# Kernel tuning notes

Measured on AMD Instinct MI355X. Metric: run time of the kernel, lower is better.

Reference implementation:

```python
import jax, jax.numpy as jnp
import numpy as np

B_, L_, H_, N_ = 8, 1024, 1024, 64

def setup_inputs() -> dict:
    key = jax.random.key(0)
    k1, k2, k3, k4 = jax.random.split(key, 4)
    return {
        "samples": jax.random.normal(k1, (B_, L_, 3 * H_), dtype=jnp.float32),
        "label_one_hot": jax.random.uniform(k2, (B_, L_, N_), dtype=jnp.float32),
        "predict": jax.random.normal(k3, (B_, L_, N_), dtype=jnp.float32),
        "W": jax.random.normal(k4, (H_, 3 * H_), dtype=jnp.float32) * (1.0 / np.sqrt(3 * H_)),
        "b_proj": jnp.zeros((H_,), dtype=jnp.float32),
    }

def reference(samples, label_one_hot, predict, W, b_proj):
    # projection: Linear(3H -> H)
    s = jnp.einsum("blk,hk->blh", samples, W) + b_proj          # [b,L,H]
    # dense similarity graph with diagonal masked out, row-softmax
    graph = jnp.einsum("blh,bmh->blm", s, s)                     # [b,L,L]
    L = graph.shape[1]
    eye = jnp.eye(L, dtype=graph.dtype)
    A = jax.nn.softmax(graph - 1e5 * eye, axis=-1)               # [b,L,L]
    # centered masked labels
    sup = label_one_hot
    row_has = (jnp.sum(sup, axis=-1) > 0.5).astype(sup.dtype)    # [b,L]
    total = jnp.sum(row_has, axis=-1)[:, None]                   # [b,1]
    avg = (jnp.sum(sup, axis=-2) / total)[:, None, :]            # [b,1,N]
    B0 = (sup - avg) * row_has[..., None]                        # [b,L,N]
    # diagonal inverse-degree scaling (elementwise, no dense diag matmul)
    d = 1.0 / (jnp.sum(A, axis=-1) + 1e-10)                      # [b,L]
    P = d[:, :, None] * jnp.swapaxes(A, -1, -2)                  # [b,L,L]
    Db = d[:, :, None] * B0                                      # [b,L,N]
    # 6-step power-iteration scan with residual injection at t==3
    ut = jnp.zeros_like(B0)
    for t in range(1, 7):
        ut = jnp.einsum("blm,bmn->bln", P, ut) + Db
        if t == 3:
            ut = ut + predict  # dropout is identity in eval mode
    return ut

if __name__ == "__main__":
    out = reference(**setup_inputs())
    print(out.shape, out.dtype)
```

## Files before the change

kernel.cpp:

```cpp
#include <hip/hip_runtime.h>


typedef _Float16 f16_t;
typedef f16_t f16x4 __attribute__((ext_vector_type(4)));
typedef f16_t f16x8 __attribute__((ext_vector_type(8)));
typedef float floatx4 __attribute__((ext_vector_type(4)));

__device__ __forceinline__ void async_copy16(const void* g, void* l) {
  __builtin_amdgcn_global_load_lds(
      (const __attribute__((address_space(1))) void*)g,
      (__attribute__((address_space(3))) void*)l, 16, 0, 0);
}

__device__ __forceinline__ f16_t hi_of(float x) { return (f16_t)x; }
__device__ __forceinline__ f16_t lo_of(float x, f16_t h) {
  return (f16_t)(x - (float)h);
}

__global__ __launch_bounds__(256) void prep_kernel(
    const float* __restrict__ W, f16_t* __restrict__ Whi, f16_t* __restrict__ Wlo,
    const float* __restrict__ samples, f16_t* __restrict__ SampH)
{
  const int bx = blockIdx.x, tid = threadIdx.x;
  if (bx < 3072) {
    const int i = bx * 256 + tid;
    float4 v = ((const float4*)W)[i];
    v.x *= 32.f; v.y *= 32.f; v.z *= 32.f; v.w *= 32.f;
    f16x4 h, l;
    f16_t h0 = hi_of(v.x); h[0] = h0; l[0] = lo_of(v.x, h0);
    f16_t h1 = hi_of(v.y); h[1] = h1; l[1] = lo_of(v.y, h1);
    f16_t h2 = hi_of(v.z); h[2] = h2; l[2] = lo_of(v.z, h2);
    f16_t h3 = hi_of(v.w); h[3] = h3; l[3] = lo_of(v.w, h3);
    *(f16x4*)(Whi + (size_t)i * 4) = h;
    *(f16x4*)(Wlo + (size_t)i * 4) = l;
  } else {
    const int i = (bx - 3072) * 256 + tid;
    const float4 v = ((const float4*)samples)[i];
    f16x4 h;
    h[0] = (f16_t)v.x; h[1] = (f16_t)v.y; h[2] = (f16_t)v.z; h[3] = (f16_t)v.w;
    *(f16x4*)(SampH + (size_t)i * 4) = h;
  }
}

struct Frags {
  f16x8 a[8];
  f16x8 bh0, bh1, bl0, bl1;
};

#define DSR(dst_, addr_, OFFSTR_) \
  asm volatile("ds_read_b128 %0, %1 offset:" OFFSTR_ : "=v"(dst_) : "v"(addr_))

__device__ __forceinline__ void read_frags_asm(unsigned sa, unsigned sb,
                                               Frags& f) {
  DSR(f.bh0, sb, "0");
  DSR(f.bh1, sb, "1024");
  DSR(f.bl0, sb, "8192");
  DSR(f.bl1, sb, "9216");
  DSR(f.a[0], sa, "0");
  DSR(f.a[1], sa, "1024");
  DSR(f.a[2], sa, "2048");
  DSR(f.a[3], sa, "3072");
  DSR(f.a[4], sa, "4096");
  DSR(f.a[5], sa, "5120");
  DSR(f.a[6], sa, "6144");
  DSR(f.a[7], sa, "7168");
}

__global__ __launch_bounds__(512, 2) void gemm1_pipe(
    const f16_t* __restrict__ Ag,
    const f16_t* __restrict__ BhG, const f16_t* __restrict__ BlG,
    const float* __restrict__ bias,
    f16_t* __restrict__ Chi, f16_t* __restrict__ Clo,
    int N, int K, float cscale)
{
  __shared__ __align__(16) char smem[131072];

  const int tid = threadIdx.x;
  const int lane = tid & 63;
  const int wave = tid >> 6;
  const int wm = wave >> 2;
  const int wn = wave & 3;
  const int m0 = blockIdx.y * 256;
  const int n0 = blockIdx.x * 128;
  const int fr = lane & 15;
  const int lch = lane >> 4;

  const int gA0 = tid;
  const int gA1 = tid + 512;
  const int rA0 = gA0 >> 2, lcA0 = (gA0 & 3) ^ ((rA0 >> 1) & 3);
  const int rA1 = gA1 >> 2, lcA1 = (gA1 & 3) ^ ((rA1 >> 1) & 3);
  const int rB = tid >> 2, lcB = (tid & 3) ^ ((rB >> 1) & 3);
  const f16_t* aSrc0 = Ag + (size_t)(m0 + rA0) * K + lcA0 * 8;
  const f16_t* aSrc1 = Ag + (size_t)(m0 + rA1) * K + lcA1 * 8;
  const f16_t* bhSrc = BhG + (size_t)(n0 + rB) * K + lcB * 8;
  const f16_t* blSrc = BlG + (size_t)(n0 + rB) * K + lcB * 8;
  char* ldsA0 = smem + gA0 * 16;
  char* ldsA1 = smem + gA1 * 16;
  char* ldsBh = smem + 16384 + (size_t)tid * 16;
  char* ldsBl = smem + 24576 + (size_t)tid * 16;

  const int swz = (lch ^ ((fr >> 1) & 3)) * 16;
  const int aoff = (wm * 128 + fr) * 64 + swz;
  const int boff = (wn * 32 + fr) * 64 + swz;
  const unsigned ldsBase =
      (unsigned)(size_t)(__attribute__((address_space(3))) char*)smem;
  const unsigned aA0 = ldsBase + (unsigned)aoff;
  const unsigned aA1 = aA0 + 32768u;
  const unsigned aA2 = aA0 + 65536u;
  const unsigned aA3 = aA0 + 98304u;
  const unsigned bA0 = ldsBase + 16384u + (unsigned)boff;
  const unsigned bA1 = bA0 + 32768u;
  const unsigned bA2 = bA0 + 65536u;
  const unsigned bA3 = bA0 + 98304u;

  floatx4 acc[8][2] = {};
  const int NS = K >> 5;

#define STAGE(SS_, SLOT_)                                     \
  do {                                                        \
    int ss = (SS_); if (ss >= NS) ss -= NS;                   \
    const int k0 = ss * 32;                                   \
    async_copy16(aSrc0 + k0, ldsA0 + (SLOT_) * 32768);        \
    async_copy16(aSrc1 + k0, ldsA1 + (SLOT_) * 32768);        \
    async_copy16(bhSrc + k0, ldsBh + (SLOT_) * 32768);        \
    async_copy16(blSrc + k0, ldsBl + (SLOT_) * 32768);        \
  } while (0)

#define MFMA8(F_, P_)                                                                                               \
  do {                                                                                                              \
    acc[2*(P_)][0]   = __builtin_amdgcn_mfma_f32_16x16x32_f16((F_).a[2*(P_)],   (F_).bh0, acc[2*(P_)][0],   0,0,0); \
    acc[2*(P_)][1]   = __builtin_amdgcn_mfma_f32_16x16x32_f16((F_).a[2*(P_)],   (F_).bh1, acc[2*(P_)][1],   0,0,0); \
    acc[2*(P_)+1][0] = __builtin_amdgcn_mfma_f32_16x16x32_f16((F_).a[2*(P_)+1], (F_).bh0, acc[2*(P_)+1][0], 0,0,0); \
    acc[2*(P_)+1][1] = __builtin_amdgcn_mfma_f32_16x16x32_f16((F_).a[2*(P_)+1], (F_).bh1, acc[2*(P_)+1][1], 0,0,0); \
    acc[2*(P_)][0]   = __builtin_amdgcn_mfma_f32_16x16x32_f16((F_).a[2*(P_)],   (F_).bl0, acc[2*(P_)][0],   0,0,0); \
    acc[2*(P_)][1]   = __builtin_amdgcn_mfma_f32_16x16x32_f16((F_).a[2*(P_)],   (F_).bl1, acc[2*(P_)][1],   0,0,0); \
    acc[2*(P_)+1][0] = __builtin_amdgcn_mfma_f32_16x16x32_f16((F_).a[2*(P_)+1], (F_).bl0, acc[2*(P_)+1][0], 0,0,0); \
    acc[2*(P_)+1][1] = __builtin_amdgcn_mfma_f32_16x16x32_f16((F_).a[2*(P_)+1], (F_).bl1, acc[2*(P_)+1][1], 0,0,0); \
  } while (0)

#define SB0 __builtin_amdgcn_sched_barrier(0)

#define HALF(SPRE_, SLOTPRE_, ARD_, BRD_, FRD_, FMM_)            \
  do {                                                           \
    STAGE(SPRE_, SLOTPRE_);                                      \
    asm volatile("s_waitcnt vmcnt(8)" ::: "memory");             \
    __builtin_amdgcn_s_barrier();                                \
    DSR(FRD_.bh0, BRD_, "0");                                    \
    DSR(FRD_.bh1, BRD_, "1024");                                 \
    DSR(FRD_.bl0, BRD_, "8192");                                 \
    SB0;                                                         \
    asm volatile("s_waitcnt lgkmcnt(3)" ::: "memory");           \
    SB0;                                                         \
    __builtin_amdgcn_s_setprio(1);                               \
    MFMA8(FMM_, 0);                                              \
    __builtin_amdgcn_s_setprio(0);                               \
    SB0;                                                         \
    DSR(FRD_.bl1, BRD_, "9216");                                 \
    DSR(FRD_.a[0], ARD_, "0");                                   \
    DSR(FRD_.a[1], ARD_, "1024");                                \
    SB0;                                                         \
    __builtin_amdgcn_s_setprio(1);                               \
    MFMA8(FMM_, 1);                                              \
    __builtin_amdgcn_s_setprio(0);                               \
    SB0;                                                         \
    DSR(FRD_.a[2], ARD_, "2048");                                \
    DSR(FRD_.a[3], ARD_, "3072");                                \
    DSR(FRD_.a[4], ARD_, "4096");                                \
    SB0;                                                         \
    __builtin_amdgcn_s_setprio(1);                               \
    MFMA8(FMM_, 2);                                              \
    __builtin_amdgcn_s_setprio(0);                               \
    SB0;                                                         \
    DSR(FRD_.a[5], ARD_, "5120");                                \
    DSR(FRD_.a[6], ARD_, "6144");                                \
    DSR(FRD_.a[7], ARD_, "7168");                                \
    SB0;                                                         \
    __builtin_amdgcn_s_setprio(1);                               \
    MFMA8(FMM_, 3);                                              \
    __builtin_amdgcn_s_setprio(0);                               \
    SB0;                                                         \
  } while (0)

  Frags f0, f1;

  STAGE(0, 0); STAGE(1, 1); STAGE(2, 2);
  asm volatile("s_waitcnt vmcnt(8)" ::: "memory");
  __builtin_amdgcn_s_barrier();
  read_frags_asm(aA0, bA0, f0);
  SB0;

  for (int s = 0; s < NS; s += 4) {
    HALF(s + 3, 3, aA1, bA1, f1, f0);
    HALF(s + 4, 0, aA2, bA2, f0, f1);
    HALF(s + 5, 1, aA3, bA3, f1, f0);
    HALF(s + 6, 2, aA0, bA0, f0, f1);
  }
  asm volatile("s_waitcnt vmcnt(0)" ::: "memory");
#undef HALF
#undef STAGE

  const int mr = (lane >> 4) * 4;
#pragma unroll
  for (int j = 0; j < 2; ++j) {
    const int n = n0 + wn * 32 + j * 16 + fr;
    const float bj = bias[n];
#pragma unroll
    for (int i = 0; i < 8; ++i) {
#pragma unroll
      for (int r = 0; r < 4; ++r) {
        const int m = m0 + wm * 128 + i * 16 + mr + r;
        float v = acc[i][j][r] * cscale + bj;
        f16_t h = hi_of(v);
        Chi[(size_t)m * N + n] = h;
        Clo[(size_t)m * N + n] = lo_of(v, h);
      }
    }
  }
}

template <int CMODE>
__global__ __launch_bounds__(256) void gemm_mfma(
    const f16_t* __restrict__ AhiG,
    const f16_t* __restrict__ BhiG, const f16_t* __restrict__ BloG,
    const float* __restrict__ bias,
    float* __restrict__ Cf, f16_t* __restrict__ Chi, f16_t* __restrict__ Clo,
    int M, int N, int K, long long sA, long long sB, long long sC, float cscale)
{
  AhiG += (long long)blockIdx.z * sA;
  BhiG += (long long)blockIdx.z * sB;
  BloG += (long long)blockIdx.z * sB;
  if (CMODE == 1) Cf += (long long)blockIdx.z * sC;

  __shared__ __align__(16) char smem[49152];
  f16_t* AsHi = (f16_t*)smem;
  f16_t* BsHi = (f16_t*)(smem + 16384);
  f16_t* BsLo = (f16_t*)(smem + 32768);

  const int tid = threadIdx.x;
  const int lane = tid & 63;
  const int wave = tid >> 6;
  const int wm = wave >> 1, wn = wave & 1;

  int m0, n0;
  if (CMODE == 0) {
    m0 = blockIdx.y * 128;
    n0 = blockIdx.x * 128;
  } else {
    int idx = blockIdx.x, i = 0, accu = 0;
    while (accu + i + 1 <= idx) { accu += i + 1; ++i; }
    m0 = i * 128;
    n0 = (idx - accu) * 128;
  }

  const int fr = lane & 15;
  const int kg = (lane >> 4) * 8;
  const int aoff = (wm * 64 + fr) * 32 + kg;
  const int boff = (wn * 64 + fr) * 32 + kg;

  floatx4 acc[4][4] = {};

  for (int k0 = 0; k0 < K; k0 += 64) {
    __syncthreads();
#pragma unroll
    for (int it = 0; it < 4; ++it) {
      const int cb = it * 256 + wave * 64;
      const int c = cb + lane;
      const int kk = c >> 9;
      const int row = (c >> 2) & 127;
      const int kc = kk * 32 + (c & 3) * 8;
      const size_t ga = (size_t)(m0 + row) * K + k0 + kc;
      const size_t gb = (size_t)(n0 + row) * K + k0 + kc;
      async_copy16(AhiG + ga, (char*)AsHi + (size_t)cb * 16);
      async_copy16(BhiG + gb, (char*)BsHi + (size_t)cb * 16);
      async_copy16(BloG + gb, (char*)BsLo + (size_t)cb * 16);
    }
    __syncthreads();

#pragma unroll
    for (int kk = 0; kk < 2; ++kk) {
      f16x8 ah[4], bh[4], bl[4];
#pragma unroll
      for (int t = 0; t < 4; ++t) {
        ah[t] = *(const f16x8*)&AsHi[kk * 4096 + aoff + t * 512];
        bh[t] = *(const f16x8*)&BsHi[kk * 4096 + boff + t * 512];
        bl[t] = *(const f16x8*)&BsLo[kk * 4096 + boff + t * 512];
      }
#pragma unroll
      for (int i = 0; i < 4; ++i)
#pragma unroll
        for (int j = 0; j < 4; ++j) {
          acc[i][j] = __builtin_amdgcn_mfma_f32_16x16x32_f16(ah[i], bh[j], acc[i][j], 0, 0, 0);
          acc[i][j] = __builtin_amdgcn_mfma_f32_16x16x32_f16(ah[i], bl[j], acc[i][j], 0, 0, 0);
        }
    }
  }

  const int mr = (lane >> 4) * 4;
#pragma unroll
  for (int j = 0; j < 4; ++j) {
    const int n = n0 + wn * 64 + j * 16 + fr;
    const float bj = (CMODE == 0) ? bias[n] : 0.f;
#pragma unroll
    for (int i = 0; i < 4; ++i) {
#pragma unroll
      for (int r = 0; r < 4; ++r) {
        const int m = m0 + wm * 64 + i * 16 + mr + r;
        float v = acc[i][j][r];
        if (CMODE == 0) {
          v = v * cscale + bj;
          f16_t h = hi_of(v);
          Chi[(size_t)m * N + n] = h;
          Clo[(size_t)m * N + n] = lo_of(v, h);
        } else {
          if (m == n) v -= 1e5f;
          Cf[(size_t)m * N + n] = v;
        }
      }
    }
  }

  if (CMODE == 1 && m0 != n0) {
    float* T = (float*)smem;
#pragma unroll
    for (int mc = 0; mc < 4; ++mc) {
      __syncthreads();
      if (wm == (mc >> 1)) {
        const int ibase = (mc & 1) * 2;
#pragma unroll
        for (int di = 0; di < 2; ++di) {
#pragma unroll
          for (int j = 0; j < 4; ++j) {
            const int nl = wn * 64 + j * 16 + fr;
#pragma unroll
            for (int r = 0; r < 4; ++r) {
              const int mloc = di * 16 + mr + r;
              T[nl * 36 + mloc] = acc[ibase + di][j][r];
            }
          }
        }
      }
      __syncthreads();
      const int row = tid >> 1, half = tid & 1;
      const float* src = &T[row * 36 + half * 16];
      float* dst = Cf + (size_t)(n0 + row) * N + m0 + mc * 32 + half * 16;
#pragma unroll
      for (int q = 0; q < 16; ++q) dst[q] = src[q];
    }
  }
}

__global__ __launch_bounds__(256) void rowstats_kernel(
    const float* __restrict__ G, float* __restrict__ mx, float* __restrict__ inv)
{
  __shared__ float red[4];
  const int tid = threadIdx.x;
  const float* g = G + (size_t)blockIdx.x * 1024;
  const float4 v = ((const float4*)g)[tid];

  float m = fmaxf(fmaxf(v.x, v.y), fmaxf(v.z, v.w));
#pragma unroll
  for (int off = 32; off > 0; off >>= 1) m = fmaxf(m, __shfl_down(m, off));
  if ((tid & 63) == 0) red[tid >> 6] = m;
  __syncthreads();
  m = fmaxf(fmaxf(red[0], red[1]), fmaxf(red[2], red[3]));
  __syncthreads();

  float s = __expf(v.x - m) + __expf(v.y - m) + __expf(v.z - m) + __expf(v.w - m);
#pragma unroll
  for (int off = 32; off > 0; off >>= 1) s += __shfl_down(s, off);
  if ((tid & 63) == 0) red[tid >> 6] = s;
  __syncthreads();
  if (tid == 0) {
    mx[blockIdx.x] = m;
    inv[blockIdx.x] = 1.0f / (red[0] + red[1] + red[2] + red[3]);
  }
}

__global__ __launch_bounds__(256) void make_at_kernel(
    const float* __restrict__ G, const float* __restrict__ mx,
    const float* __restrict__ inv, f16_t* __restrict__ At)
{
  const int row = blockIdx.x;
  const int b = row >> 10;
  const int tid = threadIdx.x;
  const float4 g = ((const float4*)(G + (size_t)row * 1024))[tid];
  const float4 m = ((const float4*)(mx + b * 1024))[tid];
  const float4 iv = ((const float4*)(inv + b * 1024))[tid];
  f16x4 o;
  o[0] = (f16_t)(__expf(g.x - m.x) * iv.x);
  o[1] = (f16_t)(__expf(g.y - m.y) * iv.y);
  o[2] = (f16_t)(__expf(g.z - m.z) * iv.z);
  o[3] = (f16_t)(__expf(g.w - m.w) * iv.w);
  *(f16x4*)(At + (size_t)row * 1024 + tid * 4) = o;
}

__global__ __launch_bounds__(1024) void make_db_kernel(
    const float* __restrict__ sup, float* __restrict__ Db, f16_t* __restrict__ DbT)
{
  const int L = 1024, Nn = 64;
  const float* s = sup + (size_t)blockIdx.x * L * Nn;
  float* db = Db + (size_t)blockIdx.x * L * Nn;
  f16_t* dbt = DbT + (size_t)blockIdx.x * L * Nn;
  __shared__ float rowhas[1024];
  __shared__ float cpart[1024];
  __shared__ float tpart[16];
  __shared__ float avg[64];
  __shared__ float totalsh;
  const int tid = threadIdx.x;

  const float4* sr = (const float4*)(s + (size_t)tid * 64);
  float ss = 0.f;
#pragma unroll
  for (int i = 0; i < 16; ++i) { const float4 v = sr[i]; ss += (v.x + v.y) + (v.z + v.w); }
  const float rh = (ss > 0.5f) ? 1.f : 0.f;
  rowhas[tid] = rh;
  float t = rh;
#pragma unroll
  for (int off = 32; off > 0; off >>= 1) t += __shfl_down(t, off);
  if ((tid & 63) == 0) tpart[tid >> 6] = t;

  const int n = tid & 63, seg = tid >> 6;
  float cs = 0.f;
  for (int l = seg * 64; l < seg * 64 + 64; ++l) cs += s[(size_t)l * 64 + n];
  cpart[seg * 64 + n] = cs;
  __syncthreads();
  if (tid == 0) { float tt = 0.f; for (int i = 0; i < 16; ++i) tt += tpart[i]; totalsh = tt; }
  __syncthreads();
  if (tid < 64) {
    float a = 0.f;
    for (int i = 0; i < 16; ++i) a += cpart[i * 64 + tid];
    avg[tid] = a / totalsh;
  }
  __syncthreads();

  const float4* s4 = (const float4*)s;
  float4* d4 = (float4*)db;
  for (int i = tid; i < (L * Nn) / 4; i += 1024) {
    float4 v = s4[i];
    const int l = i >> 4;
    const int nb = (i & 15) * 4;
    const float rhl = rowhas[l];
    v.x = (v.x - avg[nb + 0]) * rhl;
    v.y = (v.y - avg[nb + 1]) * rhl;
    v.z = (v.z - avg[nb + 2]) * rhl;
    v.w = (v.w - avg[nb + 3]) * rhl;
    d4[i] = v;
  }
  for (int i = tid; i < L * Nn; i += 1024) {
    const int n2 = i >> 10, l2 = i & 1023;
    dbt[i] = (f16_t)((s[(size_t)l2 * 64 + n2] - avg[n2]) * rowhas[l2]);
  }
}

__global__ __launch_bounds__(256) void iter_part(
    const f16_t* __restrict__ At, const f16_t* __restrict__ UT,
    float* __restrict__ Part)
{
  const int L = 1024, Nn = 64;
  const int b = blockIdx.y, l0 = blockIdx.x * 64, ks = blockIdx.z;
  At += (size_t)b * L * L;
  UT += (size_t)b * Nn * L;
  Part += (((size_t)ks * 8 + b) * L) * Nn;

  __shared__ __align__(16) f16_t AtS[2 * 64 * 32];
  __shared__ __align__(16) f16_t UtS[2 * 64 * 32];

  const int tid = threadIdx.x;
  const int lane = tid & 63;
  const int wave = tid >> 6;
  const int fr = lane & 15;
  const int kg = (lane >> 4) * 8;

  floatx4 acc[4] = {};

  for (int mi = 0; mi < 4; ++mi) {
    const int m0 = ks * 256 + mi * 64;
    __syncthreads();
#pragma unroll
    for (int it = 0; it < 2; ++it) {
      const int cb = it * 256 + wave * 64;
      const int c = cb + lane;
      const int kk = c >> 8;
      const int row = (c >> 2) & 63;
      const int kc = kk * 32 + (c & 3) * 8;
      async_copy16(At + (size_t)(l0 + row) * L + m0 + kc, (char*)AtS + (size_t)cb * 16);
      async_copy16(UT + (size_t)row * L + m0 + kc, (char*)UtS + (size_t)cb * 16);
    }
    __syncthreads();
#pragma unroll
    for (int kk = 0; kk < 2; ++kk) {
      const f16x8 a = *(const f16x8*)&AtS[kk * 2048 + (wave * 16 + fr) * 32 + kg];
#pragma unroll
      for (int j = 0; j < 4; ++j) {
        const f16x8 bf = *(const f16x8*)&UtS[kk * 2048 + (j * 16 + fr) * 32 + kg];
        acc[j] = __builtin_amdgcn_mfma_f32_16x16x32_f16(a, bf, acc[j], 0, 0, 0);
      }
    }
  }

  const int mr = (lane >> 4) * 4;
#pragma unroll
  for (int j = 0; j < 4; ++j) {
    const int n = j * 16 + fr;
#pragma unroll
    for (int r = 0; r < 4; ++r) {
      const int l = wave * 16 + mr + r;
      Part[(size_t)(l0 + l) * Nn + n] = acc[j][r];
    }
  }
}

template <int PRED, int FINAL>
__global__ __launch_bounds__(256) void iter_fin(
    const float* __restrict__ Part, const float* __restrict__ Db,
    const float* __restrict__ Pred, f16_t* __restrict__ UTn,
    float* __restrict__ OutF)
{
  const int L = 1024, Nn = 64;
  const int b = blockIdx.y, l0 = blockIdx.x * 64;
  const size_t base = ((size_t)b * L + l0) * Nn;
  const size_t ksStride = (size_t)8 * L * Nn;
  Db += base;
  if (PRED) Pred += base;

  __shared__ f16_t OutS[64 * 72];
  const int tid = threadIdx.x;

#pragma unroll
  for (int it = 0; it < 4; ++it) {
    const int idx = it * 256 + tid;
    const int l = idx >> 4, n4 = (idx & 15) * 4;
    const size_t o = (size_t)l * Nn + n4;
    float4 v = *(const float4*)(Part + base + o);
    const float4 p1 = *(const float4*)(Part + base + ksStride + o);
    const float4 p2 = *(const float4*)(Part + base + 2 * ksStride + o);
    const float4 p3 = *(const float4*)(Part + base + 3 * ksStride + o);
    v.x += p1.x; v.y += p1.y; v.z += p1.z; v.w += p1.w;
    v.x += p2.x; v.y += p2.y; v.z += p2.z; v.w += p2.w;
    v.x += p3.x; v.y += p3.y; v.z += p3.z; v.w += p3.w;
    const float4 d = *(const float4*)(Db + o);
    v.x += d.x; v.y += d.y; v.z += d.z; v.w += d.w;
    if (PRED) {
      const float4 p = *(const float4*)(Pred + o);
      v.x += p.x; v.y += p.y; v.z += p.z; v.w += p.w;
    }
    if (FINAL) {
      *(float4*)(OutF + base + o) = v;
    } else {
      OutS[(n4 + 0) * 72 + l] = (f16_t)v.x;
      OutS[(n4 + 1) * 72 + l] = (f16_t)v.y;
      OutS[(n4 + 2) * 72 + l] = (f16_t)v.z;
      OutS[(n4 + 3) * 72 + l] = (f16_t)v.w;
    }
  }
  if (!FINAL) {
    __syncthreads();
    f16_t* dst = UTn + (size_t)b * Nn * L;
#pragma unroll
    for (int it = 0; it < 2; ++it) {
      const int c = it * 256 + tid;
      const int n = c >> 3, lc = (c & 7) * 8;
      *(f16x8*)(dst + (size_t)n * L + l0 + lc) = *(const f16x8*)&OutS[n * 72 + lc];
    }
  }
}

extern "C" void kernel_launch(void* const* d_in, const int* in_sizes, int n_in,
                              void* d_out, int out_size, void* d_ws, size_t ws_size,
                              hipStream_t stream) {
  const float* samples = (const float*)d_in[0];
  const float* label   = (const float*)d_in[1];
  const float* predict = (const float*)d_in[2];
  const float* W       = (const float*)d_in[3];
  const float* bproj   = (const float*)d_in[4];
  float* out = (float*)d_out;

  char* ws = (char*)d_ws;
  f16_t* Whi = (f16_t*)ws;
  f16_t* Wlo = (f16_t*)(ws + 6291456);
  float* mx  = (float*)ws;
  float* inv = (float*)(ws + 32768);
  float* Db  = (float*)(ws + 65536);
  f16_t* DbT = (f16_t*)(ws + 65536 + 2097152);
  f16_t* UTa = (f16_t*)(ws + 65536 + 3145728);
  f16_t* UTb = (f16_t*)(ws + 65536 + 4194304);
  f16_t* SampH = (f16_t*)(ws + 12582912);
  float* G     = (float*)(ws + 12582912);
  f16_t* Shi = (f16_t*)(ws + 62914560);
  f16_t* Slo = (f16_t*)(ws + 62914560 + 16777216);
  f16_t* At  = Shi;
  float* Part = (float*)Slo;

  const long long LH = 1024LL * 1024;
  const long long LL = 1024LL * 1024;

  prep_kernel<<<dim3(27648), 256, 0, stream>>>(W, Whi, Wlo, samples, SampH);

  gemm1_pipe<<<dim3(8, 32), 512, 0, stream>>>(
      SampH, Whi, Wlo, bproj, Shi, Slo, 1024, 3072, 1.0f / 32.0f);

  gemm_mfma<1><<<dim3(36, 1, 8), 256, 0, stream>>>(
      Shi, Shi, Slo, nullptr, G, nullptr, nullptr,
      1024, 1024, 1024, LH, LH, LL, 1.0f);

  rowstats_kernel<<<8192, 256, 0, stream>>>(G, mx, inv);
  make_at_kernel<<<8192, 256, 0, stream>>>(G, mx, inv, At);

  make_db_kernel<<<8, 1024, 0, stream>>>(label, Db, DbT);

  dim3 gp(16, 8, 4), gf(16, 8);
  iter_part<<<gp, 256, 0, stream>>>(At, DbT, Part);
  iter_fin<0, 0><<<gf, 256, 0, stream>>>(Part, Db, nullptr, UTa, nullptr);
  iter_part<<<gp, 256, 0, stream>>>(At, UTa, Part);
  iter_fin<1, 0><<<gf, 256, 0, stream>>>(Part, Db, predict, UTb, nullptr);
  iter_part<<<gp, 256, 0, stream>>>(At, UTb, Part);
  iter_fin<0, 0><<<gf, 256, 0, stream>>>(Part, Db, nullptr, UTa, nullptr);
  iter_part<<<gp, 256, 0, stream>>>(At, UTa, Part);
  iter_fin<0, 0><<<gf, 256, 0, stream>>>(Part, Db, nullptr, UTb, nullptr);
  iter_part<<<gp, 256, 0, stream>>>(At, UTb, Part);
  iter_fin<0, 1><<<gf, 256, 0, stream>>>(Part, Db, nullptr, nullptr, out);
}
```

Baseline: 401.3 us.

## Fuse split-K iteration partials into single kernel with in-LDS reduction and swizzle

```diff
diff --git a/kernel.cpp b/kernel.cpp
--- a/kernel.cpp
+++ b/kernel.cpp
@@ -198,6 +198,7 @@
   asm volatile("s_waitcnt vmcnt(0)" ::: "memory");
 #undef HALF
 #undef STAGE
+#undef MFMA8
 
   const int mr = (lane >> 4) * 4;
 #pragma unroll
@@ -253,7 +254,7 @@
   }
 
   const int fr = lane & 15;
-  const int kg = (lane >> 4) * 8;
+  const int kg = ((lane >> 4) ^ ((fr >> 1) & 3)) * 8;
   const int aoff = (wm * 64 + fr) * 32 + kg;
   const int boff = (wn * 64 + fr) * 32 + kg;
 
@@ -267,7 +268,7 @@
       const int c = cb + lane;
       const int kk = c >> 9;
       const int row = (c >> 2) & 127;
-      const int kc = kk * 32 + (c & 3) * 8;
+      const int kc = kk * 32 + (((c & 3) ^ ((row >> 1) & 3)) * 8);
       const size_t ga = (size_t)(m0 + row) * K + k0 + kc;
       const size_t gb = (size_t)(n0 + row) * K + k0 + kc;
       async_copy16(AhiG + ga, (char*)AsHi + (size_t)cb * 16);
@@ -452,117 +453,175 @@
   }
 }
 
-__global__ __launch_bounds__(256) void iter_part(
+template <int PRED, int FINAL>
+__global__ __launch_bounds__(256) void iter_step(
     const f16_t* __restrict__ At, const f16_t* __restrict__ UT,
-    float* __restrict__ Part)
+    const float* __restrict__ Db, const float* __restrict__ Pred,
+    f16_t* __restrict__ UTn, float* __restrict__ OutF)
 {
   const int L = 1024, Nn = 64;
-  const int b = blockIdx.y, l0 = blockIdx.x * 64, ks = blockIdx.z;
+  const int b = blockIdx.y, l0 = blockIdx.x * 32;
   At += (size_t)b * L * L;
   UT += (size_t)b * Nn * L;
-  Part += (((size_t)ks * 8 + b) * L) * Nn;
-
-  __shared__ __align__(16) f16_t AtS[2 * 64 * 32];
-  __shared__ __align__(16) f16_t UtS[2 * 64 * 32];
+
+  __shared__ __align__(16) char smem[131072];
 
   const int tid = threadIdx.x;
   const int lane = tid & 63;
   const int wave = tid >> 6;
   const int fr = lane & 15;
-  const int kg = (lane >> 4) * 8;
-
-  floatx4 acc[4] = {};
-
-  for (int mi = 0; mi < 4; ++mi) {
-    const int m0 = ks * 256 + mi * 64;
-    __syncthreads();
-#pragma unroll
-    for (int it = 0; it < 2; ++it) {
-      const int cb = it * 256 + wave * 64;
-      const int c = cb + lane;
-      const int kk = c >> 8;
-      const int row = (c >> 2) & 63;
-      const int kc = kk * 32 + (c & 3) * 8;
-      async_copy16(At + (size_t)(l0 + row) * L + m0 + kc, (char*)AtS + (size_t)cb * 16);
-      async_copy16(UT + (size_t)row * L + m0 + kc, (char*)UtS + (size_t)cb * 16);
-    }
-    __syncthreads();
-#pragma unroll
-    for (int kk = 0; kk < 2; ++kk) {
-      const f16x8 a = *(const f16x8*)&AtS[kk * 2048 + (wave * 16 + fr) * 32 + kg];
-#pragma unroll
-      for (int j = 0; j < 4; ++j) {
-        const f16x8 bf = *(const f16x8*)&UtS[kk * 2048 + (j * 16 + fr) * 32 + kg];
-        acc[j] = __builtin_amdgcn_mfma_f32_16x16x32_f16(a, bf, acc[j], 0, 0, 0);
-      }
-    }
-  }
-
+  const int lch = lane >> 4;
+  const int mwb = wave * 256;
+
+  int g_, rw_, sc_;
+  g_ = lane;        rw_ = g_ >> 3; sc_ = (g_ & 7) ^ (rw_ & 7);
+  const f16_t* aS0 = At + (size_t)(l0 + rw_) * L + mwb + sc_ * 8;
+  g_ = lane + 64;   rw_ = g_ >> 3; sc_ = (g_ & 7) ^ (rw_ & 7);
+  const f16_t* aS1 = At + (size_t)(l0 + rw_) * L + mwb + sc_ * 8;
+  g_ = lane + 128;  rw_ = g_ >> 3; sc_ = (g_ & 7) ^ (rw_ & 7);
+  const f16_t* aS2 = At + (size_t)(l0 + rw_) * L + mwb + sc_ * 8;
+  g_ = lane + 192;  rw_ = g_ >> 3; sc_ = (g_ & 7) ^ (rw_ & 7);
+  const f16_t* aS3 = At + (size_t)(l0 + rw_) * L + mwb + sc_ * 8;
+  g_ = lane;        rw_ = g_ >> 3; sc_ = (g_ & 7) ^ (rw_ & 7);
+  const f16_t* uS0 = UT + (size_t)rw_ * L + mwb + sc_ * 8;
+  g_ = lane + 64;   rw_ = g_ >> 3; sc_ = (g_ & 7) ^ (rw_ & 7);
+  const f16_t* uS1 = UT + (size_t)rw_ * L + mwb + sc_ * 8;
+  g_ = lane + 128;  rw_ = g_ >> 3; sc_ = (g_ & 7) ^ (rw_ & 7);
+  const f16_t* uS2 = UT + (size_t)rw_ * L + mwb + sc_ * 8;
+  g_ = lane + 192;  rw_ = g_ >> 3; sc_ = (g_ & 7) ^ (rw_ & 7);
+  const f16_t* uS3 = UT + (size_t)rw_ * L + mwb + sc_ * 8;
+  g_ = lane + 256;  rw_ = g_ >> 3; sc_ = (g_ & 7) ^ (rw_ & 7);
+  const f16_t* uS4 = UT + (size_t)rw_ * L + mwb + sc_ * 8;
+  g_ = lane + 320;  rw_ = g_ >> 3; sc_ = (g_ & 7) ^ (rw_ & 7);
+  const f16_t* uS5 = UT + (size_t)rw_ * L + mwb + sc_ * 8;
+  g_ = lane + 384;  rw_ = g_ >> 3; sc_ = (g_ & 7) ^ (rw_ & 7);
+  const f16_t* uS6 = UT + (size_t)rw_ * L + mwb + sc_ * 8;
+  g_ = lane + 448;  rw_ = g_ >> 3; sc_ = (g_ & 7) ^ (rw_ & 7);
+  const f16_t* uS7 = UT + (size_t)rw_ * L + mwb + sc_ * 8;
+
+  char* stA = smem + wave * 24576;
+  char* stU = stA + 4096;
+
+  const int offK0 = fr * 128 + ((lch ^ (fr & 7)) * 16);
+  const int offK1 = fr * 128 + (((4 + lch) ^ (fr & 7)) * 16);
+
+  floatx4 acc[2][4] = {};
+
+#define STG(M0_, BUF_)                                        \
+  do {                                                        \
+    char* dA = stA + (BUF_) * 12288;                          \
+    char* dU = stU + (BUF_) * 12288;                          \
+    async_copy16(aS0 + (M0_), dA + lane * 16);                \
+    async_copy16(aS1 + (M0_), dA + 1024 + lane * 16);         \
+    async_copy16(aS2 + (M0_), dA + 2048 + lane * 16);         \
+    async_copy16(aS3 + (M0_), dA + 3072 + lane * 16);         \
+    async_copy16(uS0 + (M0_), dU + lane * 16);                \
+    async_copy16(uS1 + (M0_), dU + 1024 + lane * 16);         \
+    async_copy16(uS2 + (M0_), dU + 2048 + lane * 16);         \
+    async_copy16(uS3 + (M0_), dU + 3072 + lane * 16);         \
+    async_copy16(uS4 + (M0_), dU + 4096 + lane * 16);         \
+    async_copy16(uS5 + (M0_), dU + 5120 + lane * 16);         \
+    async_copy16(uS6 + (M0_), dU + 6144 + lane * 16);         \
+    async_copy16(uS7 + (M0_), dU + 7168 + lane * 16);         \
+  } while (0)
+
+#define LD8(b_, o_) (*(const f16x8*)((b_) + (o_)))
+#define MM(A_, U_, C_) C_ = __builtin_amdgcn_mfma_f32_16x16x32_f16(A_, U_, C_, 0, 0, 0)
+
+#define CHUNK(BUF_)                                                       \
+  do {                                                                    \
+    const char* cA = stA + (BUF_) * 12288;                                \
+    const char* cU = stU + (BUF_) * 12288;                                \
+    f16x8 a00 = LD8(cA, offK0), a01 = LD8(cA, offK1);                     \
+    f16x8 a10 = LD8(cA, offK0 + 2048), a11 = LD8(cA, offK1 + 2048);       \
+    f16x8 u00 = LD8(cU, offK0), u01 = LD8(cU, offK1);                     \
+    f16x8 u10 = LD8(cU, offK0 + 2048), u11 = LD8(cU, offK1 + 2048);       \
+    f16x8 u20 = LD8(cU, offK0 + 4096), u21 = LD8(cU, offK1 + 4096);       \
+    f16x8 u30 = LD8(cU, offK0 + 6144), u31 = LD8(cU, offK1 + 6144);       \
+    MM(a00, u00, acc[0][0]); MM(a00, u10, acc[0][1]);                     \
+    MM(a00, u20, acc[0][2]); MM(a00, u30, acc[0][3]);                     \
+    MM(a10, u00, acc[1][0]); MM(a10, u10, acc[1][1]);                     \
+    MM(a10, u20, acc[1][2]); MM(a10, u30, acc[1][3]);                     \
+    MM(a01, u01, acc[0][0]); MM(a01, u11, acc[0][1]);                     \
+    MM(a01, u21, acc[0][2]); MM(a01, u31, acc[0][3]);                     \
+    MM(a11, u01, acc[1][0]); MM(a11, u11, acc[1][1]);                     \
+    MM(a11, u21, acc[1][2]); MM(a11, u31, acc[1][3]);                     \
+  } while (0)
+
+#define SB0 __builtin_amdgcn_sched_barrier(0)
+
+  STG(0, 0);
+  STG(64, 1);
+  asm volatile("s_waitcnt vmcnt(12)" ::: "memory");
+  SB0;
+  CHUNK(0);
+  SB0;
+  STG(128, 0);
+  asm volatile("s_waitcnt vmcnt(12)" ::: "memory");
+  SB0;
+  CHUNK(1);
+  SB0;
+  STG(192, 1);
+  asm volatile("s_waitcnt vmcnt(12)" ::: "memory");
+  SB0;
+  CHUNK(0);
+  SB0;
+  asm volatile("s_waitcnt vmcnt(0)" ::: "memory");
+  SB0;
+  CHUNK(1);
+#undef CHUNK
+#undef STG
+
+  float* P = (float*)(smem + 98304) + wave * 2048;
   const int mr = (lane >> 4) * 4;
 #pragma unroll
-  for (int j = 0; j < 4; ++j) {
-    const int n = j * 16 + fr;
-#pragma unroll
-    for (int r = 0; r < 4; ++r) {
-      const int l = wave * 16 + mr + r;
-      Part[(size_t)(l0 + l) * Nn + n] = acc[j][r];
-    }
-  }
-}
-
-template <int PRED, int FINAL>
-__global__ __launch_bounds__(256) void iter_fin(
-    const float* __restrict__ Part, const float* __restrict__ Db,
-    const float* __restrict__ Pred, f16_t* __restrict__ UTn,
-    float* __restrict__ OutF)
-{
-  const int L = 1024, Nn = 64;
-  const int b = blockIdx.y, l0 = blockIdx.x * 64;
-  const size_t base = ((size_t)b * L + l0) * Nn;
-  const size_t ksStride = (size_t)8 * L * Nn;
-  Db += base;
-  if (PRED) Pred += base;
-
-  __shared__ f16_t OutS[64 * 72];
-  const int tid = threadIdx.x;
-
-#pragma unroll
-  for (int it = 0; it < 4; ++it) {
-    const int idx = it * 256 + tid;
-    const int l = idx >> 4, n4 = (idx & 15) * 4;
-    const size_t o = (size_t)l * Nn + n4;
-    float4 v = *(const float4*)(Part + base + o);
-    const float4 p1 = *(const float4*)(Part + base + ksStride + o);
-    const float4 p2 = *(const float4*)(Part + base + 2 * ksStride + o);
-    const float4 p3 = *(const float4*)(Part + base + 3 * ksStride + o);
+  for (int li = 0; li < 2; ++li)
+#pragma unroll
+    for (int j = 0; j < 4; ++j)
+#pragma unroll
+      for (int r = 0; r < 4; ++r)
+        P[(li * 16 + mr + r) * 64 + j * 16 + fr] = acc[li][j][r];
+  __syncthreads();
+
+  const float* P0 = (const float*)(smem + 98304);
+  const size_t obase = ((size_t)b * L + l0) * Nn;
+  f16_t* OutS = (f16_t*)smem;
+#pragma unroll
+  for (int it = 0; it < 2; ++it) {
+    const int e4 = it * 256 + tid;
+    const int l = e4 >> 4, n4 = (e4 & 15) * 4;
+    const int eo = l * 64 + n4;
+    float4 v = *(const float4*)(P0 + eo);
+    const float4 p1 = *(const float4*)(P0 + 2048 + eo);
+    const float4 p2 = *(const float4*)(P0 + 4096 + eo);
+    const float4 p3 = *(const float4*)(P0 + 6144 + eo);
     v.x += p1.x; v.y += p1.y; v.z += p1.z; v.w += p1.w;
     v.x += p2.x; v.y += p2.y; v.z += p2.z; v.w += p2.w;
     v.x += p3.x; v.y += p3.y; v.z += p3.z; v.w += p3.w;
-    const float4 d = *(const float4*)(Db + o);
+    const float4 d = *(const float4*)(Db + obase + eo);
     v.x += d.x; v.y += d.y; v.z += d.z; v.w += d.w;
     if (PRED) {
-      const float4 p = *(const float4*)(Pred + o);
+      const float4 p = *(const float4*)(Pred + obase + eo);
       v.x += p.x; v.y += p.y; v.z += p.z; v.w += p.w;
     }
     if (FINAL) {
-      *(float4*)(OutF + base + o) = v;
+      *(float4*)(OutF + obase + eo) = v;
     } else {
-      OutS[(n4 + 0) * 72 + l] = (f16_t)v.x;
-      OutS[(n4 + 1) * 72 + l] = (f16_t)v.y;
-      OutS[(n4 + 2) * 72 + l] = (f16_t)v.z;
-      OutS[(n4 + 3) * 72 + l] = (f16_t)v.w;
+      OutS[(n4 + 0) * 40 + l] = (f16_t)v.x;
+      OutS[(n4 + 1) * 40 + l] = (f16_t)v.y;
+      OutS[(n4 + 2) * 40 + l] = (f16_t)v.z;
+      OutS[(n4 + 3) * 40 + l] = (f16_t)v.w;
     }
   }
   if (!FINAL) {
     __syncthreads();
-    f16_t* dst = UTn + (size_t)b * Nn * L;
-#pragma unroll
-    for (int it = 0; it < 2; ++it) {
-      const int c = it * 256 + tid;
-      const int n = c >> 3, lc = (c & 7) * 8;
-      *(f16x8*)(dst + (size_t)n * L + l0 + lc) = *(const f16x8*)&OutS[n * 72 + lc];
-    }
-  }
+    f16_t* dst = UTn + (size_t)b * Nn * L + l0;
+    const int n = tid >> 2, lc = (tid & 3) * 8;
+    *(f16x8*)(dst + (size_t)n * L + lc) = *(const f16x8*)&OutS[n * 40 + lc];
+  }
+#undef SB0
+#undef LD8
+#undef MM
 }
 
 extern "C" void kernel_launch(void* const* d_in, const int* in_sizes, int n_in,
@@ -589,7 +648,6 @@
   f16_t* Shi = (f16_t*)(ws + 62914560);
   f16_t* Slo = (f16_t*)(ws + 62914560 + 16777216);
   f16_t* At  = Shi;
-  float* Part = (float*)Slo;
 
   const long long LH = 1024LL * 1024;
   const long long LL = 1024LL * 1024;
@@ -608,15 +666,10 @@
 
   make_db_kernel<<<8, 1024, 0, stream>>>(label, Db, DbT);
 
-  dim3 gp(16, 8, 4), gf(16, 8);
-  iter_part<<<gp, 256, 0, stream>>>(At, DbT, Part);
-  iter_fin<0, 0><<<gf, 256, 0, stream>>>(Part, Db, nullptr, UTa, nullptr);
-  iter_part<<<gp, 256, 0, stream>>>(At, UTa, Part);
-  iter_fin<1, 0><<<gf, 256, 0, stream>>>(Part, Db, predict, UTb, nullptr);
-  iter_part<<<gp, 256, 0, stream>>>(At, UTb, Part);
-  iter_fin<0, 0><<<gf, 256, 0, stream>>>(Part, Db, nullptr, UTa, nullptr);
-  iter_part<<<gp, 256, 0, stream>>>(At, UTa, Part);
-  iter_fin<0, 0><<<gf, 256, 0, stream>>>(Part, Db, nullptr, UTb, nullptr);
-  iter_part<<<gp, 256, 0, stream>>>(At, UTb, Part);
-  iter_fin<0, 1><<<gf, 256, 0, stream>>>(Part, Db, nullptr, nullptr, out);
-}
+  dim3 gi(32, 8);
+  iter_step<0, 0><<<gi, 256, 0, stream>>>(At, DbT, Db, nullptr, UTa, nullptr);
+  iter_step<1, 0><<<gi, 256, 0, stream>>>(At, UTa, Db, predict, UTb, nullptr);
+  iter_step<0, 0><<<gi, 256, 0, stream>>>(At, UTb, Db, nullptr, UTa, nullptr);
+  iter_step<0, 0><<<gi, 256, 0, stream>>>(At, UTa, Db, nullptr, UTb, nullptr);
+  iter_step<0, 1><<<gi, 256, 0, stream>>>(At, UTb, Db, nullptr, nullptr, out);
+}
```

Result: faster. 388.3 us (-3.2%).
